# Performance work log

Hardware: AMD Instinct MI355X
Metric: run time of the kernel (lower is better)

## Reference

```python
import jax, jax.numpy as jnp
import numpy as np

N = 16384        # num_nodes
E = 524288       # num_edges = 32 * N
F_IN = 128
F_OUT = 128


def setup_inputs() -> dict:
    key = jax.random.key(0)
    kx, kw, ks, kd = jax.random.split(key, 4)
    x = jax.random.normal(kx, (N, F_IN), dtype=jnp.float32)
    # xavier_uniform on W of shape (out, in): bound = sqrt(6/(fan_in+fan_out))
    bound = float(np.sqrt(6.0 / (F_IN + F_OUT)))
    W = jax.random.uniform(kw, (F_OUT, F_IN), jnp.float32, -bound, bound)
    B = jnp.zeros((F_OUT, F_IN), jnp.float32)  # nn.init.zeros_
    src = jax.random.randint(ks, (E,), 0, N, dtype=jnp.int32)
    # ensure every node has at least one incoming edge (avoids 1/0 = inf degree)
    dst = jnp.concatenate([jnp.arange(N, dtype=jnp.int32),
                           jax.random.randint(kd, (E - N,), 0, N, dtype=jnp.int32)])
    edge_index = jnp.stack([src, dst], axis=0)  # [2, E]; row0=source, row1=dest
    return {"x": x, "edge_index": edge_index, "W": W, "B": B}


def reference(x, edge_index, W, B):
    n = x.shape[0]
    # dense adjacency: A[i, j] = 1 iff edge j -> i (duplicates set, not add)
    A = jnp.zeros((n, n), dtype=x.dtype).at[edge_index[1], edge_index[0]].set(1.0)
    deg = jnp.sum(A, axis=1)                      # in-degree per node, [n]
    # D^-1 A x W^T + x B^T ; diag multiply expressed as row scaling
    out = ((A @ x) / deg[:, None]) @ W.T + x @ B.T
    return out
```

## Files before the change

kernel.cpp:

```cpp
#include <hip/hip_runtime.h>
#include <cstdint>
#include <cstddef>

#define NN 16384
#define FF 128
#define CAPD 96

typedef float f32x4 __attribute__((ext_vector_type(4)));
typedef short short8 __attribute__((ext_vector_type(8)));

__device__ __forceinline__ unsigned short f2bf(float f) {
    unsigned u = __float_as_uint(f);
    u += 0x7fffu + ((u >> 16) & 1u);
    return (unsigned short)(u >> 16);
}

__device__ __forceinline__ short8 ld8(const unsigned short* p) {
    return *(const short8*)p;
}

__device__ __forceinline__ float blo(unsigned v) { return __uint_as_float(v << 16); }
__device__ __forceinline__ float bhi(unsigned v) { return __uint_as_float(v & 0xffff0000u); }

__global__ __launch_bounds__(256) void k_prep(const float4* __restrict__ x,
                                              const float4* __restrict__ W,
                                              const float4* __restrict__ B,
                                              ushort4* __restrict__ xb,
                                              ushort4* __restrict__ Wb,
                                              ushort4* __restrict__ Bb,
                                              int* __restrict__ cnt) {
    int bid = blockIdx.x;
    if (bid >= 2080) {
        cnt[(bid - 2080) * 256 + threadIdx.x] = 0;
        return;
    }
    const float4* src; ushort4* dst; int i;
    if (bid < 2048)      { src = x; dst = xb; i = bid * 256 + threadIdx.x; }
    else if (bid < 2064) { src = W; dst = Wb; i = (bid - 2048) * 256 + threadIdx.x; }
    else                 { src = B; dst = Bb; i = (bid - 2064) * 256 + threadIdx.x; }
    float4 v = src[i];
    ushort4 o;
    o.x = f2bf(v.x); o.y = f2bf(v.y); o.z = f2bf(v.z); o.w = f2bf(v.w);
    dst[i] = o;
}

__global__ __launch_bounds__(256) void k_fill(const int* __restrict__ ei,
                                              int* __restrict__ cnt,
                                              unsigned short* __restrict__ slots,
                                              int E) {
    int t = blockIdx.x * 256 + threadIdx.x;
    const int4 s4 = ((const int4*)ei)[t];
    const int4 d4 = ((const int4*)(ei + E))[t];
    int sl0 = atomicAdd(&cnt[d4.x], 1);
    int sl1 = atomicAdd(&cnt[d4.y], 1);
    int sl2 = atomicAdd(&cnt[d4.z], 1);
    int sl3 = atomicAdd(&cnt[d4.w], 1);
    if (sl0 < CAPD) slots[(size_t)d4.x * CAPD + sl0] = (unsigned short)s4.x;
    if (sl1 < CAPD) slots[(size_t)d4.y * CAPD + sl1] = (unsigned short)s4.y;
    if (sl2 < CAPD) slots[(size_t)d4.z * CAPD + sl2] = (unsigned short)s4.z;
    if (sl3 < CAPD) slots[(size_t)d4.w * CAPD + sl3] = (unsigned short)s4.w;
}

__global__ __launch_bounds__(256) void k_agg(const int* __restrict__ cnt,
                                             const unsigned short* __restrict__ slots,
                                             const unsigned* __restrict__ xb,
                                             unsigned* __restrict__ aggs) {
    __shared__ unsigned bm[4][512];
    __shared__ int sl_lds[4][CAPD];
    const int w = threadIdx.x >> 6;
    const int l = threadIdx.x & 63;
    const int i = blockIdx.x * 4 + w;
#pragma unroll
    for (int j = 0; j < 8; ++j) bm[w][l + 64 * j] = 0u;
    int n = cnt[i]; if (n > CAPD) n = CAPD;
    const unsigned short* sl = slots + (size_t)i * CAPD;

    unsigned long long k0, k1;
#pragma unroll
    for (int h = 0; h < 2; ++h) {
        int j = l + 64 * h;
        bool keep = false;
        if (j < n) {
            int s = sl[j];
            sl_lds[w][j] = s;
            unsigned bit = 1u << (s & 31);
            unsigned old = atomicOr(&bm[w][s >> 5], bit);
            keep = !(old & bit);
        }
        unsigned long long m = __ballot(keep);
        if (h == 0) k0 = m; else k1 = m;
    }
    const int deg = __popcll(k0) + __popcll(k1);

    const unsigned* xbl = xb + l;
    float a0 = 0.f, a1 = 0.f;
    int j = 0;
    for (; j + 8 <= n; j += 8) {
        int s[8]; unsigned v[8];
#pragma unroll
        for (int q = 0; q < 8; ++q) s[q] = sl_lds[w][j + q];
#pragma unroll
        for (int q = 0; q < 8; ++q) v[q] = xbl[(size_t)s[q] * 64];
        unsigned bits8 = (unsigned)((j < 64 ? k0 : k1) >> (j & 63)) & 255u;
        if (bits8 == 255u) {
            a0 += blo(v[0]) + blo(v[1]) + blo(v[2]) + blo(v[3])
                + blo(v[4]) + blo(v[5]) + blo(v[6]) + blo(v[7]);
            a1 += bhi(v[0]) + bhi(v[1]) + bhi(v[2]) + bhi(v[3])
                + bhi(v[4]) + bhi(v[5]) + bhi(v[6]) + bhi(v[7]);
        } else {
#pragma unroll
            for (int q = 0; q < 8; ++q) {
                float fl = (float)((bits8 >> q) & 1u);
                a0 += fl * blo(v[q]);
                a1 += fl * bhi(v[q]);
            }
        }
    }
    for (; j < n; ++j) {
        int s = sl_lds[w][j];
        unsigned long long mm = (j < 64) ? k0 : k1;
        float fl = (float)((mm >> (j & 63)) & 1ull);
        unsigned v = xbl[(size_t)s * 64];
        a0 += fl * blo(v);
        a1 += fl * bhi(v);
    }
    float inv = 1.f / (float)deg;
    unsigned o = ((unsigned)f2bf(a1 * inv) << 16) | f2bf(a0 * inv);
    aggs[(size_t)i * 64 + l] = o;
}

__global__ __launch_bounds__(256) void k_gemm(const unsigned short* __restrict__ aggs,
                                              const unsigned short* __restrict__ xb,
                                              const unsigned short* __restrict__ Wb,
                                              const unsigned short* __restrict__ Bb,
                                              float* __restrict__ out) {
    const int bid = blockIdx.x;
    const int mb = bid >> 1, nb = bid & 1;
    const int w = threadIdx.x >> 6, l = threadIdx.x & 63;
    const int row0 = mb * 64 + w * 16;
    const int col0 = nb * 64;
    const int lr = l & 15;
    const int lk = (l >> 4) * 8;

    f32x4 acc[4];
#pragma unroll
    for (int f = 0; f < 4; ++f) acc[f] = (f32x4)0.f;

#pragma unroll
    for (int p = 0; p < 2; ++p) {
        const unsigned short* A  = p ? xb : aggs;
        const unsigned short* Wt = p ? Bb : Wb;
#pragma unroll
        for (int ks = 0; ks < 4; ++ks) {
            const int k = ks * 32 + lk;
            short8 a = ld8(&A[(size_t)(row0 + lr) * FF + k]);
#pragma unroll
            for (int f = 0; f < 4; ++f) {
                short8 b = ld8(&Wt[(size_t)(col0 + f * 16 + lr) * FF + k]);
                acc[f] = __builtin_amdgcn_mfma_f32_16x16x32_bf16(a, b, acc[f], 0, 0, 0);
            }
        }
    }
#pragma unroll
    for (int f = 0; f < 4; ++f)
#pragma unroll
        for (int r = 0; r < 4; ++r)
            out[(size_t)(row0 + (l >> 4) * 4 + r) * FF + col0 + f * 16 + lr] = acc[f][r];
}

extern "C" void kernel_launch(void* const* d_in, const int* in_sizes, int n_in,
                              void* d_out, int out_size, void* d_ws, size_t ws_size,
                              hipStream_t stream) {
    const float* x = (const float*)d_in[0];
    const int* ei = (const int*)d_in[1];
    const float* W = (const float*)d_in[2];
    const float* B = (const float*)d_in[3];
    float* out = (float*)d_out;
    const int E = in_sizes[1] / 2;

    unsigned char* ws = (unsigned char*)d_ws;
    int* cnt = (int*)ws;
    unsigned short* slots = (unsigned short*)(ws + 65536);
    unsigned* xb = (unsigned*)(ws + 3211264);
    unsigned* aggs = (unsigned*)(ws + 7405568);
    unsigned short* Wb = (unsigned short*)(ws + 11599872);
    unsigned short* Bb = (unsigned short*)(ws + 11632640);

    k_prep<<<2144, 256, 0, stream>>>((const float4*)x, (const float4*)W,
                                     (const float4*)B, (ushort4*)xb,
                                     (ushort4*)Wb, (ushort4*)Bb, cnt);
    k_fill<<<E / 4 / 256, 256, 0, stream>>>(ei, cnt, slots, E);
    k_agg<<<NN / 4, 256, 0, stream>>>(cnt, slots, xb, aggs);
    k_gemm<<<512, 256, 0, stream>>>((const unsigned short*)aggs,
                                    (const unsigned short*)xb, Wb, Bb, out);
}
```

Before: 61.87 us.

## Fuse neighbor aggregation with the projection GEMM through shared memory

Measured after the change: 75.30 us. 21.7% more time.

```diff
diff --git a/kernel.cpp b/kernel.cpp
--- a/kernel.cpp
+++ b/kernel.cpp
@@ -61,111 +61,114 @@
     if (sl3 < CAPD) slots[(size_t)d4.w * CAPD + sl3] = (unsigned short)s4.w;
 }
 
-__global__ __launch_bounds__(256) void k_agg(const int* __restrict__ cnt,
-                                             const unsigned short* __restrict__ slots,
-                                             const unsigned* __restrict__ xb,
-                                             unsigned* __restrict__ aggs) {
+__global__ __launch_bounds__(256) void k_aggemm(const int* __restrict__ cnt,
+                                                const unsigned short* __restrict__ slots,
+                                                const unsigned* __restrict__ xb,
+                                                const unsigned short* __restrict__ Wb,
+                                                const unsigned short* __restrict__ Bb,
+                                                float* __restrict__ out) {
     __shared__ unsigned bm[4][512];
     __shared__ int sl_lds[4][CAPD];
+    __shared__ unsigned agg[32 * 68];
     const int w = threadIdx.x >> 6;
     const int l = threadIdx.x & 63;
-    const int i = blockIdx.x * 4 + w;
+    const int tile = blockIdx.x;
+
+    for (int r = 0; r < 8; ++r) {
+        const int i = tile * 32 + w * 8 + r;
 #pragma unroll
-    for (int j = 0; j < 8; ++j) bm[w][l + 64 * j] = 0u;
-    int n = cnt[i]; if (n > CAPD) n = CAPD;
-    const unsigned short* sl = slots + (size_t)i * CAPD;
+        for (int j = 0; j < 8; ++j) bm[w][l + 64 * j] = 0u;
+        int n = cnt[i]; if (n > CAPD) n = CAPD;
+        const unsigned short* sl = slots + (size_t)i * CAPD;
 
-    unsigned long long k0, k1;
+        unsigned long long k0 = 0, k1 = 0;
 #pragma unroll
-    for (int h = 0; h < 2; ++h) {
-        int j = l + 64 * h;
-        bool keep = false;
-        if (j < n) {
-            int s = sl[j];
-            sl_lds[w][j] = s;
-            unsigned bit = 1u << (s & 31);
-            unsigned old = atomicOr(&bm[w][s >> 5], bit);
-            keep = !(old & bit);
+        for (int h = 0; h < 2; ++h) {
+            int j = l + 64 * h;
+            bool keep = false;
+            if (j < n) {
+                int s = sl[j];
+                sl_lds[w][j] = s;
+                unsigned bit = 1u << (s & 31);
+                unsigned old = atomicOr(&bm[w][s >> 5], bit);
+                keep = !(old & bit);
+            }
+            unsigned long long m = __ballot(keep);
+            if (h == 0) k0 = m; else k1 = m;
         }
-        unsigned long long m = __ballot(keep);
-        if (h == 0) k0 = m; else k1 = m;
-    }
-    const int deg = __popcll(k0) + __popcll(k1);
+        const int deg = __popcll(k0) + __popcll(k1);
 
-    const unsigned* xbl = xb + l;
-    float a0 = 0.f, a1 = 0.f;
-    int j = 0;
-    for (; j + 8 <= n; j += 8) {
-        int s[8]; unsigned v[8];
+        const unsigned* xbl = xb + l;
+        float a0 = 0.f, a1 = 0.f;
+        int j = 0;
+        for (; j + 8 <= n; j += 8) {
+            int s[8]; unsigned v[8];
 #pragma unroll
-        for (int q = 0; q < 8; ++q) s[q] = sl_lds[w][j + q];
+            for (int q = 0; q < 8; ++q) s[q] = sl_lds[w][j + q];
 #pragma unroll
-        for (int q = 0; q < 8; ++q) v[q] = xbl[(size_t)s[q] * 64];
-        unsigned bits8 = (unsigned)((j < 64 ? k0 : k1) >> (j & 63)) & 255u;
-        if (bits8 == 255u) {
-            a0 += blo(v[0]) + blo(v[1]) + blo(v[2]) + blo(v[3])
-                + blo(v[4]) + blo(v[5]) + blo(v[6]) + blo(v[7]);
-            a1 += bhi(v[0]) + bhi(v[1]) + bhi(v[2]) + bhi(v[3])
-                + bhi(v[4]) + bhi(v[5]) + bhi(v[6]) + bhi(v[7]);
-        } else {
+            for (int q = 0; q < 8; ++q) v[q] = xbl[(size_t)s[q] * 64];
+            unsigned bits8 = (unsigned)((j < 64 ? k0 : k1) >> (j & 63)) & 255u;
+            if (bits8 == 255u) {
+                a0 += blo(v[0]) + blo(v[1]) + blo(v[2]) + blo(v[3])
+                    + blo(v[4]) + blo(v[5]) + blo(v[6]) + blo(v[7]);
+                a1 += bhi(v[0]) + bhi(v[1]) + bhi(v[2]) + bhi(v[3])
+                    + bhi(v[4]) + bhi(v[5]) + bhi(v[6]) + bhi(v[7]);
+            } else {
 #pragma unroll
-            for (int q = 0; q < 8; ++q) {
-                float fl = (float)((bits8 >> q) & 1u);
-                a0 += fl * blo(v[q]);
-                a1 += fl * bhi(v[q]);
+                for (int q = 0; q < 8; ++q) {
+                    float fl = (float)((bits8 >> q) & 1u);
+                    a0 += fl * blo(v[q]);
+                    a1 += fl * bhi(v[q]);
+                }
             }
         }
+        for (; j < n; ++j) {
+            int s = sl_lds[w][j];
+            unsigned long long mm = (j < 64) ? k0 : k1;
+            float fl = (float)((mm >> (j & 63)) & 1ull);
+            unsigned v = xbl[(size_t)s * 64];
+            a0 += fl * blo(v);
+            a1 += fl * bhi(v);
+        }
+        float inv = 1.f / (float)deg;
+        agg[(w * 8 + r) * 68 + l] = ((unsigned)f2bf(a1 * inv) << 16) | f2bf(a0 * inv);
     }
-    for (; j < n; ++j) {
-        int s = sl_lds[w][j];
-        unsigned long long mm = (j < 64) ? k0 : k1;
-        float fl = (float)((mm >> (j & 63)) & 1ull);
-        unsigned v = xbl[(size_t)s * 64];
-        a0 += fl * blo(v);
-        a1 += fl * bhi(v);
-    }
-    float inv = 1.f / (float)deg;
-    unsigned o = ((unsigned)f2bf(a1 * inv) << 16) | f2bf(a0 * inv);
-    aggs[(size_t)i * 64 + l] = o;
-}
+    __syncthreads();
 
-__global__ __launch_bounds__(256) void k_gemm(const unsigned short* __restrict__ aggs,
-                                              const unsigned short* __restrict__ xb,
-                                              const unsigned short* __restrict__ Wb,
-                                              const unsigned short* __restrict__ Bb,
-                                              float* __restrict__ out) {
-    const int bid = blockIdx.x;
-    const int mb = bid >> 1, nb = bid & 1;
-    const int w = threadIdx.x >> 6, l = threadIdx.x & 63;
-    const int row0 = mb * 64 + w * 16;
-    const int col0 = nb * 64;
+    const int row0g = tile * 32 + (w >> 1) * 16;
+    const int row0l = (w >> 1) * 16;
+    const int col0 = (w & 1) * 64;
     const int lr = l & 15;
-    const int lk = (l >> 4) * 8;
+    const int lq = l >> 4;
+    const unsigned short* xbs = (const unsigned short*)xb;
 
     f32x4 acc[4];
 #pragma unroll
     for (int f = 0; f < 4; ++f) acc[f] = (f32x4)0.f;
 
 #pragma unroll
-    for (int p = 0; p < 2; ++p) {
-        const unsigned short* A  = p ? xb : aggs;
-        const unsigned short* Wt = p ? Bb : Wb;
+    for (int ks = 0; ks < 4; ++ks) {
+        short8 a = *(const short8*)&agg[(row0l + lr) * 68 + ks * 16 + lq * 4];
 #pragma unroll
-        for (int ks = 0; ks < 4; ++ks) {
-            const int k = ks * 32 + lk;
-            short8 a = ld8(&A[(size_t)(row0 + lr) * FF + k]);
+        for (int f = 0; f < 4; ++f) {
+            short8 b = ld8(&Wb[(size_t)(col0 + f * 16 + lr) * FF + ks * 32 + lq * 8]);
+            acc[f] = __builtin_amdgcn_mfma_f32_16x16x32_bf16(a, b, acc[f], 0, 0, 0);
+        }
+    }
 #pragma unroll
-            for (int f = 0; f < 4; ++f) {
-                short8 b = ld8(&Wt[(size_t)(col0 + f * 16 + lr) * FF + k]);
-                acc[f] = __builtin_amdgcn_mfma_f32_16x16x32_bf16(a, b, acc[f], 0, 0, 0);
-            }
+    for (int ks = 0; ks < 4; ++ks) {
+        short8 a = ld8(&xbs[(size_t)(row0g + lr) * FF + ks * 32 + lq * 8]);
+#pragma unroll
+        for (int f = 0; f < 4; ++f) {
+            short8 b = ld8(&Bb[(size_t)(col0 + f * 16 + lr) * FF + ks * 32 + lq * 8]);
+            acc[f] = __builtin_amdgcn_mfma_f32_16x16x32_bf16(a, b, acc[f], 0, 0, 0);
         }
     }
 #pragma unroll
     for (int f = 0; f < 4; ++f)
 #pragma unroll
-        for (int r = 0; r < 4; ++r)
-            out[(size_t)(row0 + (l >> 4) * 4 + r) * FF + col0 + f * 16 + lr] = acc[f][r];
+        for (int r4 = 0; r4 < 4; ++r4)
+            out[(size_t)(row0g + lq * 4 + r4) * FF + col0 + f * 16 + lr] = acc[f][r4];
 }
 
 extern "C" void kernel_launch(void* const* d_in, const int* in_sizes, int n_in,
@@ -182,15 +185,12 @@
     int* cnt = (int*)ws;
     unsigned short* slots = (unsigned short*)(ws + 65536);
     unsigned* xb = (unsigned*)(ws + 3211264);
-    unsigned* aggs = (unsigned*)(ws + 7405568);
-    unsigned short* Wb = (unsigned short*)(ws + 11599872);
-    unsigned short* Bb = (unsigned short*)(ws + 11632640);
+    unsigned short* Wb = (unsigned short*)(ws + 7405568);
+    unsigned short* Bb = (unsigned short*)(ws + 7438336);
 
     k_prep<<<2144, 256, 0, stream>>>((const float4*)x, (const float4*)W,
                                      (const float4*)B, (ushort4*)xb,
                                      (ushort4*)Wb, (ushort4*)Bb, cnt);
     k_fill<<<E / 4 / 256, 256, 0, stream>>>(ei, cnt, slots, E);
-    k_agg<<<NN / 4, 256, 0, stream>>>(cnt, slots, xb, aggs);
-    k_gemm<<<512, 256, 0, stream>>>((const unsigned short*)aggs,
-                                    (const unsigned short*)xb, Wb, Bb, out);
+    k_aggemm<<<NN / 32, 256, 0, stream>>>(cnt, slots, xb, Wb, Bb, out);
 }
```
